# Kernel optimization log

Measured on AMD Instinct MI355X. Metric: run time of the kernel, lower is better.

Reference implementation:

```python
import jax, jax.numpy as jnp
import numpy as np

HEADS = 16
KEY_SIZE = 64
HEAD_SIZE = 64
D_MODEL = 1024
MASK_BIG = 1e12


def setup_inputs() -> dict:
    key = jax.random.key(0)
    ks = jax.random.split(key, 16)
    B, S, D = 4, 2048, D_MODEL
    qk_dim = HEADS * KEY_SIZE
    out_dim = HEADS * HEAD_SIZE
    s = 0.02
    return {
        'q': jax.random.normal(ks[0], (B, S, D), jnp.float32),
        'k': jax.random.normal(ks[1], (B, S, D), jnp.float32),
        'v': jax.random.normal(ks[2], (B, S, D), jnp.float32),
        'q_mask': jax.random.randint(ks[3], (B, S), 0, 2, jnp.int32),
        'v_mask': jax.random.randint(ks[4], (B, S), 0, 2, jnp.int32),
        'Wq': jax.random.normal(ks[5], (D, qk_dim), jnp.float32) * s,
        'bq': jnp.zeros((qk_dim,), jnp.float32),
        'Wk': jax.random.normal(ks[6], (D, qk_dim), jnp.float32) * s,
        'bk': jnp.zeros((qk_dim,), jnp.float32),
        'Wv': jax.random.normal(ks[7], (D, out_dim), jnp.float32) * s,
        'bv': jnp.zeros((out_dim,), jnp.float32),
        'Wo': jax.random.normal(ks[8], (out_dim, out_dim), jnp.float32) * s,
        'bo': jnp.zeros((out_dim,), jnp.float32),
    }


def reference(q, k, v, q_mask, v_mask, Wq, bq, Wk, bk, Wv, bv, Wo, bo):
    B, Sq, _ = q.shape
    Sk = k.shape[1]
    # projections -> [B, H, S, d]
    qw = (q @ Wq + bq).reshape(B, Sq, HEADS, KEY_SIZE).transpose(0, 2, 1, 3)
    kw = (k @ Wk + bk).reshape(B, Sk, HEADS, KEY_SIZE).transpose(0, 2, 1, 3)
    vw = (v @ Wv + bv).reshape(B, Sk, HEADS, HEAD_SIZE).transpose(0, 2, 1, 3)
    # scaled dot-product scores [B, H, Sq, Sk]
    a = jnp.einsum('bhqd,bhkd->bhqk', qw, kw) / np.sqrt(KEY_SIZE).astype(np.float32)
    # v_mask: additive -inf-like penalty on padded keys (mode=1, axis=-1)
    vm = v_mask.astype(a.dtype)[:, None, None, :]
    a = a - (1.0 - vm) * MASK_BIG
    # a_mask=True: causal mask (mask future positions)
    causal = jnp.tril(jnp.ones((Sq, Sk), a.dtype))
    a = a - (1.0 - causal) * MASK_BIG
    a = jax.nn.softmax(a, axis=-1)
    # attention output [B, Sq, H*head_size]
    o = jnp.einsum('bhqk,bhkd->bhqd', a, vw).transpose(0, 2, 1, 3).reshape(B, Sq, HEADS * HEAD_SIZE)
    o = o @ Wo + bo
    # q_mask: multiplicative zeroing of padded query outputs (mode=0, axis=1)
    o = o * q_mask.astype(o.dtype)[:, :, None]
    return o
```

## Files before the change

### kernel.cpp

```cpp
#include <hip/hip_runtime.h>
#include <hip/hip_bf16.h>

typedef __attribute__((ext_vector_type(8))) short v8s;
typedef __attribute__((ext_vector_type(4))) float v4f;
typedef __attribute__((ext_vector_type(16))) float v16f;
typedef __attribute__((ext_vector_type(4))) unsigned v4u;

#define S_LEN 2048
#define NB 4
#define NH 16
#define LOG2E 1.4426950408889634f
#define CMASK 1443109011456.0f
#define DEFER_THR 11.55f

__device__ __forceinline__ short f2bf(float f) {
    __hip_bfloat16 h = __float2bfloat16(f);
    union { __hip_bfloat16 h; short s; } u; u.h = h; return u.s;
}

__device__ __forceinline__ unsigned cvtpk(float lo, float hi) {
    unsigned r;
    asm("v_cvt_pk_bf16_f32 %0, %1, %2" : "=v"(r) : "v"(lo), "v"(hi));
    return r;
}

__device__ __forceinline__ int swz(int row, int col) {
    return (row * 128 + col) ^ ((row & 7) << 4);
}

__device__ __forceinline__ void async16(void* lds, const void* g) {
    __builtin_amdgcn_global_load_lds(
        (const __attribute__((address_space(1))) unsigned int*)g,
        (__attribute__((address_space(3))) unsigned int*)lds, 16, 0, 0);
}

#define MFMA16(a, b, c) __builtin_amdgcn_mfma_f32_16x16x32_bf16((a), (b), (c), 0, 0, 0)
#define MFMA32(a, b, c) __builtin_amdgcn_mfma_f32_32x32x16_bf16((a), (b), (c), 0, 0, 0)

__global__ __launch_bounds__(256) void convert_all(const float* __restrict__ q,
                                                   const float* __restrict__ k,
                                                   const float* __restrict__ v,
                                                   short* __restrict__ Xq,
                                                   short* __restrict__ Xk,
                                                   short* __restrict__ Xv,
                                                   float* __restrict__ outz) {
    if (blockIdx.y == 3) {
        size_t i = ((size_t)blockIdx.x * 256 + threadIdx.x) * 8;
        float4 z4 = {0.f, 0.f, 0.f, 0.f};
        *(float4*)(outz + i) = z4;
        *(float4*)(outz + i + 4) = z4;
        return;
    }
    const float* in = (blockIdx.y == 0) ? q : (blockIdx.y == 1) ? k : v;
    short* out = (blockIdx.y == 0) ? Xq : (blockIdx.y == 1) ? Xk : Xv;
    size_t i = ((size_t)blockIdx.x * 256 + threadIdx.x) * 8;
    float4 a = *(const float4*)(in + i);
    float4 b = *(const float4*)(in + i + 4);
    v8s o;
    o[0] = f2bf(a.x); o[1] = f2bf(a.y); o[2] = f2bf(a.z); o[3] = f2bf(a.w);
    o[4] = f2bf(b.x); o[5] = f2bf(b.y); o[6] = f2bf(b.z); o[7] = f2bf(b.w);
    *(v8s*)(out + i) = o;
}

__global__ __launch_bounds__(256) void build_pen(const int* __restrict__ vm,
                                                 short* __restrict__ penC) {
    int i = blockIdx.x * 256 + threadIdx.x;
    penC[i] = vm[i] ? (short)0 : f2bf(-CMASK);
}

__global__ __launch_bounds__(256) void compact_qmask(const int* __restrict__ qm,
                                                     int* __restrict__ idx,
                                                     int* __restrict__ nq) {
    const int b = blockIdx.x;
    const int* m = qm + b * S_LEN;
    int* ib = idx + b * S_LEN;
    __shared__ int cnt[256];
    const int t = threadIdx.x;
    int loc[8], c = 0;
#pragma unroll
    for (int i = 0; i < 8; ++i) { int s = t * 8 + i; if (m[s]) loc[c++] = s; }
    cnt[t] = c;
    __syncthreads();
    for (int d = 1; d < 256; d <<= 1) {
        int v = (t >= d) ? cnt[t - d] : 0;
        __syncthreads();
        cnt[t] += v;
        __syncthreads();
    }
    int off = cnt[t] - c;
    for (int i = 0; i < c; ++i) ib[off + i] = loc[i];
    if (t == 255) nq[b] = cnt[255];
}

__global__ __launch_bounds__(256) void transpose_all(const float* __restrict__ Wq,
                                                     const float* __restrict__ Wk,
                                                     const float* __restrict__ Wv,
                                                     const float* __restrict__ Wo,
                                                     short* __restrict__ WTq,
                                                     short* __restrict__ WTk,
                                                     short* __restrict__ WTv,
                                                     short* __restrict__ WTo) {
    const int z = blockIdx.z;
    const float* W = (z == 0) ? Wq : (z == 1) ? Wk : (z == 2) ? Wv : Wo;
    short* WT = (z == 0) ? WTq : (z == 1) ? WTk : (z == 2) ? WTv : WTo;
    __shared__ float tile[32][33];
    int k0 = blockIdx.x * 32, n0 = blockIdx.y * 32;
    int tx = threadIdx.x & 31, ty = threadIdx.x >> 5;
#pragma unroll
    for (int i = 0; i < 4; ++i)
        tile[ty + i * 8][tx] = W[(size_t)(k0 + ty + i * 8) * 1024 + n0 + tx];
    __syncthreads();
#pragma unroll
    for (int i = 0; i < 4; ++i)
        WT[(size_t)(n0 + ty + i * 8) * 1024 + k0 + tx] = f2bf(tile[tx][ty + i * 8]);
}

__global__ __launch_bounds__(256)
void proj_all(const short* __restrict__ Xk, const short* __restrict__ Xv,
              const short* __restrict__ Xq,
              const short* __restrict__ WTk, const short* __restrict__ WTv,
              const short* __restrict__ WTq,
              const float* __restrict__ bk, const float* __restrict__ bv,
              const float* __restrict__ bq,
              const int* __restrict__ idx, const int* __restrict__ nq,
              short* __restrict__ KW, short* __restrict__ VT,
              short* __restrict__ QW) {
    __shared__ short As[128 * 64];
    __shared__ short Bs[128 * 64];
    const int tid = threadIdx.x;
    const int l = tid & 63, w = tid >> 6;
    const int g = l >> 4, ql = l & 15;
    const int z = blockIdx.z;
    const int bid = blockIdx.x;
    const int y = (bid & 7) + 8 * (bid >> 6);
    const int n0 = ((bid >> 3) & 7) * 128;
    const int wr = w >> 1, wc = w & 1;

    int b = 0, m0 = y * 128, m0c = 0, nqv = 0;
    const int* idxb = nullptr;
    if (z == 2) {
        if (y >= 36) return;
        b = y / 9; m0c = (y % 9) * 128;
        nqv = nq[b];
        if (m0c >= nqv) return;
        idxb = idx + b * S_LEN;
    }
    const short* A  = (z == 0) ? Xk : (z == 1) ? Xv : Xq;
    const short* BT = (z == 0) ? WTk : (z == 1) ? WTv : WTq;
    const float* bias = (z == 0) ? bk : (z == 1) ? bv : bq;

    int arow[4];
#pragma unroll
    for (int i = 0; i < 4; ++i) {
        int row = (i * 256 + tid) >> 3;
        if (z == 2) {
            int jc = m0c + row;
            arow[i] = b * S_LEN + idxb[(jc < nqv) ? jc : (nqv - 1)];
        } else {
            arow[i] = m0 + row;
        }
    }
    const int c8 = (((l & 7) ^ (l >> 3))) * 8;

    v4f acc[4][4] = {};

    for (int kt = 0; kt < 16; ++kt) {
        const int kk = kt * 64;
        __syncthreads();
#pragma unroll
        for (int i = 0; i < 4; ++i) {
            int ci = i * 256 + tid;
            async16((char*)As + (size_t)(i * 256 + w * 64) * 16,
                    A + (size_t)arow[i] * 1024 + kk + c8);
            async16((char*)Bs + (size_t)(i * 256 + w * 64) * 16,
                    BT + (size_t)(n0 + (ci >> 3)) * 1024 + kk + c8);
        }
        __syncthreads();
#pragma unroll
        for (int ks = 0; ks < 2; ++ks) {
            v8s af[4], bfr[4];
#pragma unroll
            for (int mt = 0; mt < 4; ++mt)
                af[mt] = *(const v8s*)((char*)As +
                          swz(wr * 64 + mt * 16 + ql, ks * 64 + g * 16));
#pragma unroll
            for (int nt = 0; nt < 4; ++nt)
                bfr[nt] = *(const v8s*)((char*)Bs +
                          swz(wc * 64 + nt * 16 + ql, ks * 64 + g * 16));
#pragma unroll
            for (int mt = 0; mt < 4; ++mt)
#pragma unroll
                for (int nt = 0; nt < 4; ++nt)
                    acc[mt][nt] = MFMA16(af[mt], bfr[nt], acc[mt][nt]);
        }
    }

#pragma unroll
    for (int nt = 0; nt < 4; ++nt) {
        int col = n0 + wc * 64 + nt * 16 + ql;
        float bval = bias[col];
        int hh = col >> 6, dd = col & 63;
#pragma unroll
        for (int mt = 0; mt < 4; ++mt) {
#pragma unroll
            for (int r = 0; r < 4; ++r) {
                int lrow = wr * 64 + mt * 16 + g * 4 + r;
                float vv = acc[mt][nt][r] + bval;
                if (z == 0) {
                    int gm = m0 + lrow;
                    int bb = gm >> 11, ss = gm & 2047;
                    KW[((size_t)(bb * NH + hh) * S_LEN + ss) * 64 + dd] = f2bf(vv);
                } else if (z == 1) {
                    int gm = m0 + lrow;
                    int bb = gm >> 11, ss = gm & 2047;
                    VT[((size_t)(bb * NH + hh) * 64 + dd) * S_LEN + ss] = f2bf(vv);
                } else {
                    int jc = m0c + lrow;
                    vv *= 0.125f * LOG2E;
                    QW[((size_t)(b * NH + hh) * S_LEN + jc) * 64 + dd] = f2bf(vv);
                }
            }
        }
    }
}

__global__ __launch_bounds__(64)
void attn_kernel(const short* __restrict__ QW, const short* __restrict__ KW,
                 const short* __restrict__ VT, const short* __restrict__ penC,
                 const int* __restrict__ idx, const int* __restrict__ nq,
                 short* __restrict__ O) {
    const int l = threadIdx.x;
    const int lq = l & 31, hi = l >> 5;
    const int bh = blockIdx.x;
    const int chunk = 63 - (int)blockIdx.y;
    const int b = bh >> 4, hd = bh & 15;

    const int nqv = nq[b];
    const int cy = chunk * 32;
    if (cy >= nqv) return;

    const short* Qp = QW + (size_t)bh * S_LEN * 64;
    const short* Kp = KW + (size_t)bh * S_LEN * 64;
    const short* Vp = VT + (size_t)bh * 64 * S_LEN;
    const short* pp = penC + b * S_LEN;
    const int* idxb = idx + b * S_LEN;

    const int j = cy + lq;
    const int jj = (j < nqv) ? j : (nqv - 1);
    const int q_glob = idxb[jj];
    const int qmin = __builtin_amdgcn_readfirstlane(q_glob);

    int lastj = cy + 31; if (lastj > nqv - 1) lastj = nqv - 1;
    const int NT = (idxb[lastj] >> 6) + 1;

    v8s qf[4];
#pragma unroll
    for (int ks = 0; ks < 4; ++ks)
        qf[ks] = *(const v8s*)(Qp + (size_t)jj * 64 + ks * 16 + hi * 8);
    v8s qf4 = {};
    qf4[0] = hi ? (short)0 : (short)0x3F80;

    v16f accO[2] = {};
    float m_run = -INFINITY, l_run = 0.f;

    auto tile = [&](int kt, bool causal) {
        const int k0 = kt * 64;
        const short* kb = Kp + (size_t)(k0 + lq) * 64 + hi * 8;
        const short* vb = Vp + (size_t)lq * S_LEN + k0 + hi * 8;
        short p0 = pp[k0 + lq], p1 = pp[k0 + lq + 32];

        v8s kf0[4], kf1[4];
#pragma unroll
        for (int ks = 0; ks < 4; ++ks) {
            kf0[ks] = *(const v8s*)(kb + ks * 16);
            kf1[ks] = *(const v8s*)(kb + 32 * 64 + ks * 16);
        }
        v16f acc0 = {}, acc1 = {};
        __builtin_amdgcn_s_setprio(1);
#pragma unroll
        for (int ks = 0; ks < 4; ++ks) {
            acc0 = MFMA32(kf0[ks], qf[ks], acc0);
            acc1 = MFMA32(kf1[ks], qf[ks], acc1);
        }
        v8s k4a = {}, k4b = {};
        k4a[0] = hi ? (short)0 : p0;
        k4b[0] = hi ? (short)0 : p1;
        acc0 = MFMA32(k4a, qf4, acc0);
        acc1 = MFMA32(k4b, qf4, acc1);
        __builtin_amdgcn_s_setprio(0);

        float s[32];
#pragma unroll
        for (int jn = 0; jn < 16; ++jn) { s[jn] = acc0[jn]; s[16 + jn] = acc1[jn]; }
        if (causal) {
#pragma unroll
            for (int t = 0; t < 2; ++t)
#pragma unroll
                for (int jn = 0; jn < 16; ++jn) {
                    int kp = k0 + t * 32 + (jn & 3) + 8 * (jn >> 2) + 4 * hi;
                    if (kp > q_glob) s[t * 16 + jn] -= CMASK;
                }
        }
        float t8[8];
#pragma unroll
        for (int i = 0; i < 8; ++i)
            t8[i] = fmaxf(fmaxf(s[i], s[i + 8]), fmaxf(s[i + 16], s[i + 24]));
#pragma unroll
        for (int i = 0; i < 4; ++i) t8[i] = fmaxf(t8[i], t8[i + 4]);
        float tmax = fmaxf(fmaxf(t8[0], t8[1]), fmaxf(t8[2], t8[3]));
        tmax = fmaxf(tmax, __shfl_xor(tmax, 32, 64));

        if (__any(tmax > m_run + DEFER_THR)) {
            float mnew = fmaxf(m_run, tmax);
            float scale = exp2f(m_run - mnew);
            m_run = mnew;
            l_run *= scale;
#pragma unroll
            for (int jn = 0; jn < 16; ++jn) {
                float sc = __shfl(scale, (jn & 3) + 8 * (jn >> 2) + 4 * hi, 64);
                accO[0][jn] *= sc;
                accO[1][jn] *= sc;
            }
        }
#pragma unroll
        for (int i = 0; i < 32; ++i) s[i] = exp2f(s[i] - m_run);
        float u8[8];
#pragma unroll
        for (int i = 0; i < 8; ++i)
            u8[i] = (s[i] + s[i + 8]) + (s[i + 16] + s[i + 24]);
#pragma unroll
        for (int i = 0; i < 4; ++i) u8[i] += u8[i + 4];
        float psum = (u8[0] + u8[1]) + (u8[2] + u8[3]);
        psum += __shfl_xor(psum, 32, 64);
        l_run += psum;

        v8s vf0[4], vf1[4];
#pragma unroll
        for (int ks = 0; ks < 4; ++ks) {
            vf0[ks] = *(const v8s*)(vb + ks * 16);
            vf1[ks] = *(const v8s*)(vb + 32 * S_LEN + ks * 16);
        }

        v8s PA[4];
#pragma unroll
        for (int t = 0; t < 2; ++t)
#pragma unroll
            for (int sf = 0; sf < 2; ++sf) {
                int base = t * 16 + sf * 8;
                unsigned x0 = cvtpk(s[base + 0], s[base + 1]);
                unsigned x1 = cvtpk(s[base + 2], s[base + 3]);
                unsigned y0 = cvtpk(s[base + 4], s[base + 5]);
                unsigned y1 = cvtpk(s[base + 6], s[base + 7]);
                asm volatile("v_permlane32_swap_b32 %0, %1" : "+v"(x0), "+v"(y0));
                asm volatile("v_permlane32_swap_b32 %0, %1" : "+v"(x1), "+v"(y1));
                v4u wv; wv[0] = x0; wv[1] = x1; wv[2] = y0; wv[3] = y1;
                union { v4u u; v8s s8; } cvt; cvt.u = wv;
                PA[t * 2 + sf] = cvt.s8;
            }

        __builtin_amdgcn_s_setprio(1);
#pragma unroll
        for (int ks = 0; ks < 4; ++ks) {
            accO[0] = MFMA32(PA[ks], vf0[ks], accO[0]);
            accO[1] = MFMA32(PA[ks], vf1[ks], accO[1]);
        }
        __builtin_amdgcn_s_setprio(0);
    };

    for (int kt = 0; kt < NT; ++kt)
        tile(kt, kt * 64 + 63 > qmin);

    int kt = NT;
    while (kt < 32 && __any(m_run < -1e11f)) {
        tile(kt, true);
        ++kt;
    }

    float inv = 1.0f / l_run;
#pragma unroll
    for (int jn = 0; jn < 16; ++jn) {
        int rowq = (jn & 3) + 8 * (jn >> 2) + 4 * hi;
        float iv = __shfl(inv, rowq, 64);
        int jrow = cy + rowq;
        if (jrow < nqv) {
            size_t base = (size_t)(b * S_LEN + jrow) * 1024 + hd * 64 + lq;
            O[base]      = f2bf(accO[0][jn] * iv);
            O[base + 32] = f2bf(accO[1][jn] * iv);
        }
    }
}

__global__ __launch_bounds__(256)
void out_gemm_c(const short* __restrict__ A, const short* __restrict__ BT,
                const float* __restrict__ bias, const int* __restrict__ idx,
                const int* __restrict__ nq, float* __restrict__ out) {
    __shared__ short As[128 * 64];
    __shared__ short Bs[128 * 64];
    const int tid = threadIdx.x;
    const int l = tid & 63, w = tid >> 6;
    const int g = l >> 4, ql = l & 15;
    const int bid = blockIdx.x;
    const int y = (bid & 7) + 8 * (bid >> 6);
    if (y >= 36) return;
    const int n0 = ((bid >> 3) & 7) * 128;
    const int b = y / 9;
    const int m0c = (y % 9) * 128;
    const int nqv = nq[b];
    if (m0c >= nqv) return;
    const int* idxb = idx + b * S_LEN;
    const int wr = w >> 1, wc = w & 1;
    const int c8 = (((l & 7) ^ (l >> 3))) * 8;

    v4f acc[4][4] = {};

    for (int kt = 0; kt < 16; ++kt) {
        const int kk = kt * 64;
        __syncthreads();
#pragma unroll
        for (int i = 0; i < 4; ++i) {
            int ci = i * 256 + tid;
            int row = ci >> 3;
            async16((char*)As + (size_t)(i * 256 + w * 64) * 16,
                    A + (size_t)(b * S_LEN + m0c + row) * 1024 + kk + c8);
            async16((char*)Bs + (size_t)(i * 256 + w * 64) * 16,
                    BT + (size_t)(n0 + row) * 1024 + kk + c8);
        }
        __syncthreads();
#pragma unroll
        for (int ks = 0; ks < 2; ++ks) {
            v8s af[4], bfr[4];
#pragma unroll
            for (int mt = 0; mt < 4; ++mt)
                af[mt] = *(const v8s*)((char*)As +
                          swz(wr * 64 + mt * 16 + ql, ks * 64 + g * 16));
#pragma unroll
            for (int nt = 0; nt < 4; ++nt)
                bfr[nt] = *(const v8s*)((char*)Bs +
                          swz(wc * 64 + nt * 16 + ql, ks * 64 + g * 16));
#pragma unroll
            for (int mt = 0; mt < 4; ++mt)
#pragma unroll
                for (int nt = 0; nt < 4; ++nt)
                    acc[mt][nt] = MFMA16(af[mt], bfr[nt], acc[mt][nt]);
        }
    }

#pragma unroll
    for (int nt = 0; nt < 4; ++nt) {
        int col = n0 + wc * 64 + nt * 16 + ql;
        float bval = bias[col];
#pragma unroll
        for (int mt = 0; mt < 4; ++mt) {
#pragma unroll
            for (int r = 0; r < 4; ++r) {
                int jc = m0c + wr * 64 + mt * 16 + g * 4 + r;
                if (jc < nqv) {
                    int orig = idxb[jc];
                    out[(size_t)(b * S_LEN + orig) * 1024 + col] =
                        acc[mt][nt][r] + bval;
                }
            }
        }
    }
}

extern "C" void kernel_launch(void* const* d_in, const int* in_sizes, int n_in,
                              void* d_out, int out_size, void* d_ws, size_t ws_size,
                              hipStream_t stream) {
    (void)in_sizes; (void)n_in; (void)out_size; (void)ws_size;
    const float* q  = (const float*)d_in[0];
    const float* k  = (const float*)d_in[1];
    const float* v  = (const float*)d_in[2];
    const int* qmask = (const int*)d_in[3];
    const int* vmask = (const int*)d_in[4];
    const float* Wq = (const float*)d_in[5];
    const float* bq = (const float*)d_in[6];
    const float* Wk = (const float*)d_in[7];
    const float* bk = (const float*)d_in[8];
    const float* Wv = (const float*)d_in[9];
    const float* bv = (const float*)d_in[10];
    const float* Wo = (const float*)d_in[11];
    const float* bo = (const float*)d_in[12];
    float* out = (float*)d_out;

    char* ws = (char*)d_ws;
    const size_t MB = 1024 * 1024;
    short* Xq  = (short*)(ws + 0 * MB);
    short* Xk  = (short*)(ws + 16 * MB);
    short* Xv  = (short*)(ws + 32 * MB);
    short* WTq = (short*)(ws + 48 * MB);
    short* WTk = (short*)(ws + 50 * MB);
    short* WTv = (short*)(ws + 52 * MB);
    short* WTo = (short*)(ws + 54 * MB);
    short* QW  = (short*)(ws + 56 * MB);
    short* KW  = (short*)(ws + 72 * MB);
    short* VTb = (short*)(ws + 88 * MB);
    short* Ob  = (short*)(ws + 104 * MB);
    short* penC = (short*)(ws + 120 * MB);
    int* idxB  = (int*)(ws + 121 * MB);
    int* nqB   = (int*)(ws + 122 * MB);

    convert_all<<<dim3(4096, 4), 256, 0, stream>>>(q, k, v, Xq, Xk, Xv, out);
    transpose_all<<<dim3(32, 32, 4), 256, 0, stream>>>(Wq, Wk, Wv, Wo,
                                                       WTq, WTk, WTv, WTo);
    build_pen<<<32, 256, 0, stream>>>(vmask, penC);
    compact_qmask<<<NB, 256, 0, stream>>>(qmask, idxB, nqB);

    proj_all<<<dim3(512, 1, 3), 256, 0, stream>>>(Xk, Xv, Xq, WTk, WTv, WTq,
                                                  bk, bv, bq, idxB, nqB,
                                                  KW, VTb, QW);
    attn_kernel<<<dim3(64, 64), 64, 0, stream>>>(QW, KW, VTb, penC, idxB, nqB, Ob);
    out_gemm_c<<<320, 256, 0, stream>>>(Ob, WTo, bo, idxB, nqB, out);
}
```

Measured before the change: 246.6 us.

## Split long causal attention chunks into two KV pieces with a combine kernel

Query chunks whose causal key range covers more than 8 tiles are split into two halves along the key dimension, each handled by its own workgroup. Each half writes its running max, running sum and bf16 partial accumulator to scratch space reused from dead input buffers. A new combine kernel merges the two halves with log-sum-exp rescaling. This is meant to even out the long tail of heavy causal blocks and raise occupancy, at the cost of an extra launch, partial-result memory traffic and bf16 rounding of the partials. Split blocks also skip the deferred fully-masked-row fallback loop.

Result: slower. 289.7 us (+17.5%).

```diff
diff --git a/kernel.cpp b/kernel.cpp
--- a/kernel.cpp
+++ b/kernel.cpp
@@ -16,6 +16,10 @@
 __device__ __forceinline__ short f2bf(float f) {
     __hip_bfloat16 h = __float2bfloat16(f);
     union { __hip_bfloat16 h; short s; } u; u.h = h; return u.s;
+}
+__device__ __forceinline__ float bf2f(short s) {
+    union { unsigned u; float f; } u; u.u = ((unsigned)(unsigned short)s) << 16;
+    return u.f;
 }
 
 __device__ __forceinline__ unsigned cvtpk(float lo, float hi) {
@@ -228,11 +232,15 @@
 void attn_kernel(const short* __restrict__ QW, const short* __restrict__ KW,
                  const short* __restrict__ VT, const short* __restrict__ penC,
                  const int* __restrict__ idx, const int* __restrict__ nq,
-                 short* __restrict__ O) {
+                 short* __restrict__ O,
+                 float* __restrict__ mP, float* __restrict__ lP,
+                 short* __restrict__ accP) {
     const int l = threadIdx.x;
     const int lq = l & 31, hi = l >> 5;
     const int bh = blockIdx.x;
-    const int chunk = 63 - (int)blockIdx.y;
+    const int y = blockIdx.y;
+    const int piece = y & 1;
+    const int chunk = 63 - (y >> 1);
     const int b = bh >> 4, hd = bh & 15;
 
     const int nqv = nq[b];
@@ -252,6 +260,11 @@
 
     int lastj = cy + 31; if (lastj > nqv - 1) lastj = nqv - 1;
     const int NT = (idxb[lastj] >> 6) + 1;
+    const bool split = (NT > 8);
+    if (!split && piece) return;
+    const int H = NT >> 1;
+    const int t0 = split ? (piece ? H : 0) : 0;
+    const int t1 = split ? (piece ? NT : H) : NT;
 
     v8s qf[4];
 #pragma unroll
@@ -367,10 +380,26 @@
         __builtin_amdgcn_s_setprio(0);
     };
 
-    for (int kt = 0; kt < NT; ++kt)
+    for (int kt = t0; kt < t1; ++kt)
         tile(kt, kt * 64 + 63 > qmin);
 
-    int kt = NT;
+    if (split) {
+        const int pidx = (bh * 64 + chunk) * 2 + piece;
+        if (hi == 0) {
+            mP[(size_t)pidx * 32 + lq] = m_run;
+            lP[(size_t)pidx * 32 + lq] = l_run;
+        }
+        short* aPp = accP + (size_t)pidx * 2048;
+#pragma unroll
+        for (int jn = 0; jn < 16; ++jn) {
+            int rowq = (jn & 3) + 8 * (jn >> 2) + 4 * hi;
+            aPp[rowq * 64 + lq]      = f2bf(accO[0][jn]);
+            aPp[rowq * 64 + 32 + lq] = f2bf(accO[1][jn]);
+        }
+        return;
+    }
+
+    int kt = t1;
     while (kt < 32 && __any(m_run < -1e11f)) {
         tile(kt, true);
         ++kt;
@@ -387,6 +416,40 @@
             O[base]      = f2bf(accO[0][jn] * iv);
             O[base + 32] = f2bf(accO[1][jn] * iv);
         }
+    }
+}
+
+__global__ __launch_bounds__(64)
+void attn_combine(const float* __restrict__ mP, const float* __restrict__ lP,
+                  const short* __restrict__ accP, const int* __restrict__ idx,
+                  const int* __restrict__ nq, short* __restrict__ O) {
+    const int bh = blockIdx.x, chunk = blockIdx.y;
+    const int b = bh >> 4, hd = bh & 15;
+    const int nqv = nq[b];
+    const int cy = chunk * 32;
+    if (cy >= nqv) return;
+    const int* idxb = idx + b * S_LEN;
+    int lastj = cy + 31; if (lastj > nqv - 1) lastj = nqv - 1;
+    const int NT = (idxb[lastj] >> 6) + 1;
+    if (NT <= 8) return;
+
+    const int lane = threadIdx.x;
+    const int p0 = (bh * 64 + chunk) * 2;
+    const float* m0 = mP + (size_t)p0 * 32;  const float* m1 = m0 + 32;
+    const float* l0 = lP + (size_t)p0 * 32;  const float* l1 = l0 + 32;
+    const short* a0 = accP + (size_t)p0 * 2048;
+    const short* a1 = a0 + 2048;
+
+    for (int r = 0; r < 32; ++r) {
+        int jrow = cy + r;
+        if (jrow >= nqv) break;
+        float ma = m0[r], mb = m1[r];
+        float m = fmaxf(ma, mb);
+        float s0 = exp2f(ma - m), s1 = exp2f(mb - m);
+        float lsum = l0[r] * s0 + l1[r] * s1;
+        float o = (bf2f(a0[r * 64 + lane]) * s0 + bf2f(a1[r * 64 + lane]) * s1)
+                  / lsum;
+        O[(size_t)(b * S_LEN + jrow) * 1024 + hd * 64 + lane] = f2bf(o);
     }
 }
 
@@ -499,6 +562,9 @@
     short* penC = (short*)(ws + 120 * MB);
     int* idxB  = (int*)(ws + 121 * MB);
     int* nqB   = (int*)(ws + 122 * MB);
+    short* accP = (short*)(ws + 0 * MB);
+    float* mP   = (float*)(ws + 34 * MB);
+    float* lP   = (float*)(ws + 37 * MB);
 
     convert_all<<<dim3(4096, 4), 256, 0, stream>>>(q, k, v, Xq, Xk, Xv, out);
     transpose_all<<<dim3(32, 32, 4), 256, 0, stream>>>(Wq, Wk, Wv, Wo,
@@ -509,6 +575,8 @@
     proj_all<<<dim3(512, 1, 3), 256, 0, stream>>>(Xk, Xv, Xq, WTk, WTv, WTq,
                                                   bk, bv, bq, idxB, nqB,
                                                   KW, VTb, QW);
-    attn_kernel<<<dim3(64, 64), 64, 0, stream>>>(QW, KW, VTb, penC, idxB, nqB, Ob);
+    attn_kernel<<<dim3(64, 128), 64, 0, stream>>>(QW, KW, VTb, penC, idxB, nqB,
+                                                  Ob, mP, lP, accP);
+    attn_combine<<<dim3(64, 64), 64, 0, stream>>>(mP, lP, accP, idxB, nqB, Ob);
     out_gemm_c<<<320, 256, 0, stream>>>(Ob, WTo, bo, idxB, nqB, out);
 }
```
